# Performance work log

Hardware: AMD Instinct MI355X
Metric: run time of the kernel (lower is better)

## Reference

```python
import jax, jax.numpy as jnp
import numpy as np

MAX_PTS_NORM = 10.0


def setup_inputs() -> dict:
    key = jax.random.key(0)
    k1, k2, k3, k4, k5, k6, k7 = jax.random.split(key, 7)
    N, M, C = 200000, 32, 4
    features = jax.random.normal(k1, (N, M, C), dtype=jnp.float32)
    num_points = jax.random.randint(k2, (N,), 0, 33, dtype=jnp.int64)
    coors = jax.random.randint(k3, (N, 4), 0, 400, dtype=jnp.int64)
    # MLP params: Linear(5,16) -> ReLU -> Linear(16,1)
    W1 = jax.random.normal(k4, (5, 16), dtype=jnp.float32) * (1.0 / np.sqrt(5))
    b1 = jax.random.normal(k5, (16,), dtype=jnp.float32) * 0.01
    W2 = jax.random.normal(k6, (16, 1), dtype=jnp.float32) * (1.0 / np.sqrt(16))
    b2 = jax.random.normal(k7, (1,), dtype=jnp.float32) * 0.01
    return {"features": features, "num_points": num_points, "coors": coors,
            "W1": W1, "b1": b1, "W2": W2, "b2": b2}


def reference(features, num_points, coors, W1, b1, W2, b2):
    N, M, C = features.shape
    npf = num_points.astype(jnp.float32)
    p_density = (jnp.clip(npf, None, MAX_PTS_NORM) / MAX_PTS_NORM)[:, None]  # (N,1)
    xyz = features[:, :, :3]  # (N,M,3)
    mask = (jnp.arange(M)[None, :] < num_points[:, None]).astype(jnp.float32)[:, :, None]  # (N,M,1)
    denom = jnp.clip(npf, 1.0, None)[:, None]  # (N,1)
    sum_xyz = jnp.sum(xyz * mask, axis=1)  # (N,3)
    mean_xyz = sum_xyz / denom  # (N,3)
    diff = (xyz - mean_xyz[:, None, :]) * mask  # (N,M,3)
    var_xyz = jnp.sum(diff * diff, axis=1) / denom  # (N,3)
    var_xyz_mean = jnp.mean(var_xyz, axis=1, keepdims=True)  # (N,1)
    p_var = jnp.exp(-0.5 * var_xyz_mean)  # (N,1)
    mlp_input = jnp.concatenate([p_density, p_var, mean_xyz], axis=1)  # (N,5)
    h = jax.nn.relu(mlp_input @ W1 + b1)  # (N,16)
    logits = h @ W2 + b2  # (N,1)
    return jax.nn.sigmoid(logits)
```

## Files before the change

### kernel.cpp

```cpp
#include <hip/hip_runtime.h>
#include <math.h>


typedef float floatx4 __attribute__((ext_vector_type(4)));

#define LANES_PER_VOX 4
#define VOX_PER_BLOCK 64

__global__ __launch_bounds__(256) void vfe_kernel(
    const floatx4* __restrict__ feats,
    const int*    __restrict__ num_points,
    const float*  __restrict__ W1,
    const float*  __restrict__ b1,
    const float*  __restrict__ W2,
    const float*  __restrict__ b2,
    float*        __restrict__ out,
    int N)
{
    __shared__ float sW1[80];
    __shared__ float sb1[16];
    __shared__ float sW2[16];
    __shared__ float sb2;

    const int t = threadIdx.x;
    if (t < 80) sW1[t] = W1[t];
    if (t < 16) { sb1[t] = b1[t]; sW2[t] = W2[t]; }
    if (t == 0) sb2 = b2[0];
    __syncthreads();

    const int j   = t & 3;
    const int vox = blockIdx.x * VOX_PER_BLOCK + (t >> 2);
    if (vox >= N) return;

    const int   np        = num_points[vox];
    const float npf       = (float)np;
    const float inv_denom = 1.0f / fmaxf(npf, 1.0f);

    const floatx4* vbase = feats + (size_t)vox * 32;
    floatx4 f[8];
    #pragma unroll
    for (int i = 0; i < 8; ++i)
        f[i] = __builtin_nontemporal_load(&vbase[j + 4 * i]);

    float sx = 0.0f, sy = 0.0f, sz = 0.0f, sq = 0.0f;
    #pragma unroll
    for (int i = 0; i < 8; ++i) {
        const float m = (j + 4 * i < np) ? 1.0f : 0.0f;
        sx += f[i].x * m;
        sy += f[i].y * m;
        sz += f[i].z * m;
        sq += m * (f[i].x * f[i].x + f[i].y * f[i].y + f[i].z * f[i].z);
    }

    #pragma unroll
    for (int d = 1; d <= 2; d <<= 1) {
        sx += __shfl_xor(sx, d);
        sy += __shfl_xor(sy, d);
        sz += __shfl_xor(sz, d);
        sq += __shfl_xor(sq, d);
    }

    const float mean_x = sx * inv_denom;
    const float mean_y = sy * inv_denom;
    const float mean_z = sz * inv_denom;

    float qtot = sq - (sx * sx + sy * sy + sz * sz) * inv_denom;
    float var_mean = fmaxf(qtot, 0.0f) * inv_denom * (1.0f / 3.0f);

    const float p_var     = __expf(-0.5f * var_mean);
    const float p_density = fminf(npf, 10.0f) * 0.1f;

    float c = 0.0f;
    #pragma unroll
    for (int u0 = 0; u0 < 16; u0 += 4) {
        const int u = u0 + j;
        float h = sb1[u]
                + p_density * sW1[u]
                + p_var     * sW1[16 + u]
                + mean_x    * sW1[32 + u]
                + mean_y    * sW1[48 + u]
                + mean_z    * sW1[64 + u];
        c += fmaxf(h, 0.0f) * sW2[u];
    }
    c += __shfl_xor(c, 1);
    c += __shfl_xor(c, 2);

    if (j == 0) {
        const float logit = c + sb2;
        out[vox] = 1.0f / (1.0f + __expf(-logit));
    }
}

extern "C" void kernel_launch(void* const* d_in, const int* in_sizes, int n_in,
                              void* d_out, int out_size, void* d_ws, size_t ws_size,
                              hipStream_t stream) {
    const floatx4* feats     = (const floatx4*)d_in[0];
    const int*    num_points = (const int*)d_in[1];
    const float*  W1 = (const float*)d_in[3];
    const float*  b1 = (const float*)d_in[4];
    const float*  W2 = (const float*)d_in[5];
    const float*  b2 = (const float*)d_in[6];
    float* out = (float*)d_out;

    const int N = in_sizes[1];
    const int blocks = (N + VOX_PER_BLOCK - 1) / VOX_PER_BLOCK;
    vfe_kernel<<<blocks, 256, 0, stream>>>(feats, num_points, W1, b1, W2, b2, out, N);
}
```

Baseline: 154.5 us.

## Remap voxels so each wave loads contiguous 1KB rows per half-wave

Each wave now handles 16 voxels, with each half-wave of 32 lanes reading one full voxel row per iteration, so a single load instruction covers a contiguous region instead of a strided lane-to-point layout. Per-voxel sums are reduced with 5-step butterfly shuffles across 32 lanes, eight times, and one lane per voxel then runs the full 16-unit MLP serially. Loads should coalesce better, but reduction shuffle traffic grows substantially and the MLP work is concentrated on a quarter of the lanes.

```diff
diff --git a/kernel.cpp b/kernel.cpp
--- a/kernel.cpp
+++ b/kernel.cpp
@@ -4,7 +4,8 @@
 
 typedef float floatx4 __attribute__((ext_vector_type(4)));
 
-#define LANES_PER_VOX 4
+#define VOX_PER_WAVE 16
+#define WAVES_PER_BLOCK 4
 #define VOX_PER_BLOCK 64
 
 __global__ __launch_bounds__(256) void vfe_kernel(
@@ -28,66 +29,88 @@
     if (t == 0) sb2 = b2[0];
     __syncthreads();
 
-    const int j   = t & 3;
-    const int vox = blockIdx.x * VOX_PER_BLOCK + (t >> 2);
-    if (vox >= N) return;
+    const int lane = t & 63;
+    const int wave = t >> 6;
+    const int h    = lane >> 5;
+    const int p    = lane & 31;
+    const int tile = (blockIdx.x * WAVES_PER_BLOCK + wave) * VOX_PER_WAVE;
+    if (tile >= N) return;
 
-    const int   np        = num_points[vox];
-    const float npf       = (float)np;
-    const float inv_denom = 1.0f / fmaxf(npf, 1.0f);
+    const floatx4* base = feats + (size_t)tile * 32;
 
-    const floatx4* vbase = feats + (size_t)vox * 32;
     floatx4 f[8];
-    #pragma unroll
-    for (int i = 0; i < 8; ++i)
-        f[i] = __builtin_nontemporal_load(&vbase[j + 4 * i]);
+    int     npv[8];
+    const bool full = (tile + VOX_PER_WAVE <= N);
+    if (full) {
+        #pragma unroll
+        for (int i = 0; i < 8; ++i)
+            f[i] = __builtin_nontemporal_load(&base[i * 64 + lane]);
+        #pragma unroll
+        for (int i = 0; i < 8; ++i)
+            npv[i] = num_points[tile + 2 * i + h];
+    } else {
+        #pragma unroll
+        for (int i = 0; i < 8; ++i) {
+            const int v = tile + 2 * i + h;
+            if (v < N) {
+                f[i]   = base[i * 64 + lane];
+                npv[i] = num_points[v];
+            } else {
+                f[i]   = (floatx4){0.0f, 0.0f, 0.0f, 0.0f};
+                npv[i] = 0;
+            }
+        }
+    }
 
-    float sx = 0.0f, sy = 0.0f, sz = 0.0f, sq = 0.0f;
+    float KX = 0.0f, KY = 0.0f, KZ = 0.0f, KQ = 0.0f;
+    int   KNP = 0;
+
     #pragma unroll
     for (int i = 0; i < 8; ++i) {
-        const float m = (j + 4 * i < np) ? 1.0f : 0.0f;
-        sx += f[i].x * m;
-        sy += f[i].y * m;
-        sz += f[i].z * m;
-        sq += m * (f[i].x * f[i].x + f[i].y * f[i].y + f[i].z * f[i].z);
+        const float m  = (p < npv[i]) ? 1.0f : 0.0f;
+        float sx = f[i].x * m;
+        float sy = f[i].y * m;
+        float sz = f[i].z * m;
+        float sq = m * (f[i].x * f[i].x + f[i].y * f[i].y + f[i].z * f[i].z);
+        #pragma unroll
+        for (int d = 1; d <= 16; d <<= 1) {
+            sx += __shfl_xor(sx, d);
+            sy += __shfl_xor(sy, d);
+            sz += __shfl_xor(sz, d);
+            sq += __shfl_xor(sq, d);
+        }
+        if (p == i) { KX = sx; KY = sy; KZ = sz; KQ = sq; KNP = npv[i]; }
     }
 
-    #pragma unroll
-    for (int d = 1; d <= 2; d <<= 1) {
-        sx += __shfl_xor(sx, d);
-        sy += __shfl_xor(sy, d);
-        sz += __shfl_xor(sz, d);
-        sq += __shfl_xor(sq, d);
-    }
+    if (p < 8) {
+        const int vox = tile + 2 * p + h;
+        if (vox < N) {
+            const float npf       = (float)KNP;
+            const float inv_denom = 1.0f / fmaxf(npf, 1.0f);
 
-    const float mean_x = sx * inv_denom;
-    const float mean_y = sy * inv_denom;
-    const float mean_z = sz * inv_denom;
+            const float mean_x = KX * inv_denom;
+            const float mean_y = KY * inv_denom;
+            const float mean_z = KZ * inv_denom;
 
-    float qtot = sq - (sx * sx + sy * sy + sz * sz) * inv_denom;
-    float var_mean = fmaxf(qtot, 0.0f) * inv_denom * (1.0f / 3.0f);
+            const float qtot     = KQ - (KX * KX + KY * KY + KZ * KZ) * inv_denom;
+            const float var_mean = fmaxf(qtot, 0.0f) * inv_denom * (1.0f / 3.0f);
 
-    const float p_var     = __expf(-0.5f * var_mean);
-    const float p_density = fminf(npf, 10.0f) * 0.1f;
+            const float p_var     = __expf(-0.5f * var_mean);
+            const float p_density = fminf(npf, 10.0f) * 0.1f;
 
-    float c = 0.0f;
-    #pragma unroll
-    for (int u0 = 0; u0 < 16; u0 += 4) {
-        const int u = u0 + j;
-        float h = sb1[u]
-                + p_density * sW1[u]
-                + p_var     * sW1[16 + u]
-                + mean_x    * sW1[32 + u]
-                + mean_y    * sW1[48 + u]
-                + mean_z    * sW1[64 + u];
-        c += fmaxf(h, 0.0f) * sW2[u];
-    }
-    c += __shfl_xor(c, 1);
-    c += __shfl_xor(c, 2);
-
-    if (j == 0) {
-        const float logit = c + sb2;
-        out[vox] = 1.0f / (1.0f + __expf(-logit));
+            float c = sb2;
+            #pragma unroll
+            for (int u = 0; u < 16; ++u) {
+                float hu = sb1[u]
+                         + p_density * sW1[u]
+                         + p_var     * sW1[16 + u]
+                         + mean_x    * sW1[32 + u]
+                         + mean_y    * sW1[48 + u]
+                         + mean_z    * sW1[64 + u];
+                c += fmaxf(hu, 0.0f) * sW2[u];
+            }
+            out[vox] = 1.0f / (1.0f + __expf(-c));
+        }
     }
 }
 
```

Measured after the change: 168.5 us. +9.1%, slower.

## Stage voxel features through swizzled LDS with fully coalesced wave loads

Applied to the files above, without the earlier changes.

Each wave now loads a contiguous 16-voxel tile of features with lane-contiguous 16-byte loads, fully coalesced, and writes them into a swizzled shared-memory buffer. Threads then read their strided points from LDS instead of global memory. The aim is better global coalescing than the old j+4*i strided pattern. The cost is 32KB of LDS per block, which can limit occupancy, plus an extra LDS round trip. Previously each quad of lanes already read a contiguous 512B span, so access was already largely coalesced.

```diff
diff --git a/kernel.cpp b/kernel.cpp
--- a/kernel.cpp
+++ b/kernel.cpp
@@ -4,7 +4,6 @@
 
 typedef float floatx4 __attribute__((ext_vector_type(4)));
 
-#define LANES_PER_VOX 4
 #define VOX_PER_BLOCK 64
 
 __global__ __launch_bounds__(256) void vfe_kernel(
@@ -17,6 +16,7 @@
     float*        __restrict__ out,
     int N)
 {
+    __shared__ floatx4 sfeat[VOX_PER_BLOCK * 32];
     __shared__ float sW1[80];
     __shared__ float sb1[16];
     __shared__ float sW2[16];
@@ -26,30 +26,60 @@
     if (t < 80) sW1[t] = W1[t];
     if (t < 16) { sb1[t] = b1[t]; sW2[t] = W2[t]; }
     if (t == 0) sb2 = b2[0];
+
+    const int lane = t & 63;
+    const int wave = t >> 6;
+    const int tileVox = blockIdx.x * VOX_PER_BLOCK;
+    const int wtile   = tileVox + wave * 16;
+
+    floatx4* slds = sfeat + wave * 16 * 32;
+
+    floatx4 val[8];
+    if (wtile + 16 <= N) {
+        #pragma unroll
+        for (int i = 0; i < 8; ++i)
+            val[i] = __builtin_nontemporal_load(
+                        feats + ((size_t)wtile * 32 + i * 64 + lane));
+    } else {
+        #pragma unroll
+        for (int i = 0; i < 8; ++i) {
+            const int e = i * 64 + lane;
+            val[i] = (floatx4){0.0f, 0.0f, 0.0f, 0.0f};
+            if (wtile + (e >> 5) < N)
+                val[i] = feats[(size_t)wtile * 32 + e];
+        }
+    }
+    #pragma unroll
+    for (int i = 0; i < 8; ++i) {
+        const int e = i * 64 + lane;
+        const int v = e >> 5;
+        const int p = e & 31;
+        slds[v * 32 + (p ^ ((v & 1) << 2))] = val[i];
+    }
     __syncthreads();
 
-    const int j   = t & 3;
-    const int vox = blockIdx.x * VOX_PER_BLOCK + (t >> 2);
+    const int j    = t & 3;
+    const int vloc = t >> 2;
+    const int vox  = tileVox + vloc;
     if (vox >= N) return;
 
     const int   np        = num_points[vox];
     const float npf       = (float)np;
     const float inv_denom = 1.0f / fmaxf(npf, 1.0f);
 
-    const floatx4* vbase = feats + (size_t)vox * 32;
-    floatx4 f[8];
-    #pragma unroll
-    for (int i = 0; i < 8; ++i)
-        f[i] = __builtin_nontemporal_load(&vbase[j + 4 * i]);
+    const floatx4* vrow = sfeat + vloc * 32;
+    const int      swz  = (vloc & 1) << 2;
 
     float sx = 0.0f, sy = 0.0f, sz = 0.0f, sq = 0.0f;
     #pragma unroll
     for (int i = 0; i < 8; ++i) {
-        const float m = (j + 4 * i < np) ? 1.0f : 0.0f;
-        sx += f[i].x * m;
-        sy += f[i].y * m;
-        sz += f[i].z * m;
-        sq += m * (f[i].x * f[i].x + f[i].y * f[i].y + f[i].z * f[i].z);
+        const int p = j + 4 * i;
+        const floatx4 f = vrow[p ^ swz];
+        const float m = (p < np) ? 1.0f : 0.0f;
+        sx += f.x * m;
+        sy += f.y * m;
+        sz += f.z * m;
+        sq += m * (f.x * f.x + f.y * f.y + f.z * f.z);
     }
 
     #pragma unroll
@@ -64,8 +94,8 @@
     const float mean_y = sy * inv_denom;
     const float mean_z = sz * inv_denom;
 
-    float qtot = sq - (sx * sx + sy * sy + sz * sz) * inv_denom;
-    float var_mean = fmaxf(qtot, 0.0f) * inv_denom * (1.0f / 3.0f);
+    const float qtot     = sq - (sx * sx + sy * sy + sz * sz) * inv_denom;
+    const float var_mean = fmaxf(qtot, 0.0f) * inv_denom * (1.0f / 3.0f);
 
     const float p_var     = __expf(-0.5f * var_mean);
     const float p_density = fminf(npf, 10.0f) * 0.1f;
```

Measured after the change: 155.9 us. About the same (+0.9%).
